# Kernel optimization log

Hardware: AMD Instinct MI355X
Metric: run time of the kernel (lower is better)

Reference implementation:

```python
import jax, jax.numpy as jnp
import numpy as np

N_NODES = 50000
N_EDGES = 800000
IN_CH, HIDDEN, OUT_CH = 128, 128, 64
EPS = 1e-5


def setup_inputs() -> dict:
    key = jax.random.key(0)
    ks = jax.random.split(key, 16)
    s = lambda fan_in: 1.0 / np.sqrt(fan_in)
    return {
        "x": jax.random.normal(ks[0], (N_NODES, IN_CH), dtype=jnp.float32),
        "edge_index": jax.random.randint(ks[1], (2, N_EDGES), 0, N_NODES, dtype=jnp.int64),
        # SAGEConv1: lin_l (neighbors, with bias), lin_r (root, no bias)
        "Wl1": jax.random.uniform(ks[2], (HIDDEN, IN_CH), jnp.float32, -s(IN_CH), s(IN_CH)),
        "bl1": jnp.zeros((HIDDEN,), jnp.float32),
        "Wr1": jax.random.uniform(ks[3], (HIDDEN, IN_CH), jnp.float32, -s(IN_CH), s(IN_CH)),
        # SAGEConv2
        "Wl2": jax.random.uniform(ks[4], (HIDDEN, HIDDEN), jnp.float32, -s(HIDDEN), s(HIDDEN)),
        "bl2": jnp.zeros((HIDDEN,), jnp.float32),
        "Wr2": jax.random.uniform(ks[5], (HIDDEN, HIDDEN), jnp.float32, -s(HIDDEN), s(HIDDEN)),
        # SAGEConv3
        "Wl3": jax.random.uniform(ks[6], (OUT_CH, HIDDEN), jnp.float32, -s(HIDDEN), s(HIDDEN)),
        "bl3": jnp.zeros((OUT_CH,), jnp.float32),
        "Wr3": jax.random.uniform(ks[7], (OUT_CH, HIDDEN), jnp.float32, -s(HIDDEN), s(HIDDEN)),
        # LayerNorms
        "g1": jnp.ones((HIDDEN,), jnp.float32),
        "beta1": jnp.zeros((HIDDEN,), jnp.float32),
        "g2": jnp.ones((HIDDEN,), jnp.float32),
        "beta2": jnp.zeros((HIDDEN,), jnp.float32),
    }


def _sage_conv(x, src, dst, n_nodes, Wl, bl, Wr):
    # mean aggregation of source features at target nodes (PyG SAGEConv, aggr='mean')
    msg = x[src]                                             # [E, C] gather
    sums = jax.ops.segment_sum(msg, dst, num_segments=n_nodes)
    cnt = jax.ops.segment_sum(jnp.ones((src.shape[0],), x.dtype), dst, num_segments=n_nodes)
    mean = sums / jnp.maximum(cnt, 1.0)[:, None]
    return mean @ Wl.T + bl + x @ Wr.T


def _layernorm(h, g, b):
    mu = jnp.mean(h, axis=-1, keepdims=True)
    var = jnp.mean(jnp.square(h - mu), axis=-1, keepdims=True)
    return (h - mu) * jax.lax.rsqrt(var + EPS) * g + b


def reference(x, edge_index, Wl1, bl1, Wr1, Wl2, bl2, Wr2, Wl3, bl3, Wr3, g1, beta1, g2, beta2):
    src, dst = edge_index[0], edge_index[1]
    n = x.shape[0]
    h = jax.nn.relu(_sage_conv(x, src, dst, n, Wl1, bl1, Wr1))
    h = _layernorm(h, g1, beta1)
    h = jax.nn.relu(_sage_conv(h, src, dst, n, Wl2, bl2, Wr2))
    h = _layernorm(h, g2, beta2)
    return _sage_conv(h, src, dst, n, Wl3, bl3, Wr3)
```

## Files before the change

kernel.cpp:

```cpp
#include <hip/hip_runtime.h>

#define NNODES 50000
#define NEDGES 800000
#define FILL_CHUNK 7168
#define FILL_NCHUNK 112
#define FILL_BLOCKS (FILL_NCHUNK * 8)
#define GEMM_BLOCKS ((NNODES + 127) / 128)
#define CAP 96

using bf16x8  = __attribute__((ext_vector_type(8))) __bf16;
using floatx4 = __attribute__((ext_vector_type(4))) float;

__device__ __forceinline__ float bf2f(unsigned short u) {
  unsigned int v = ((unsigned int)u) << 16;
  return __builtin_bit_cast(float, v);
}
__device__ __forceinline__ unsigned short f2bf(float f) {
  unsigned int u = __builtin_bit_cast(unsigned int, f);
  u += 0x7fffu + ((u >> 16) & 1u);
  return (unsigned short)(u >> 16);
}

__device__ __forceinline__ signed char enc_i8(float f) {
  float g = fminf(fmaxf(f * 32.0f, -127.0f), 127.0f);
  return (signed char)__float2int_rn(g);
}

struct WPtrs {
  const float* src[6];
  unsigned short* dst[6];
  int n[6];
};

__global__ __launch_bounds__(256) void convw_zero_kernel(WPtrs p, int* __restrict__ cnt) {
  if (blockIdx.x < 320) {
    int i = blockIdx.x * 256 + threadIdx.x;
#pragma unroll
    for (int s = 0; s < 6; ++s) {
      if (i < p.n[s]) {
        p.dst[s][i] = f2bf(p.src[s][i]);
        return;
      }
      i -= p.n[s];
    }
  } else {
    int i = (blockIdx.x - 320) * 256 + threadIdx.x;
    if (i < NNODES) cnt[i] = 0;
  }
}

__device__ __forceinline__ void fill_body(int bid, const int* __restrict__ src,
                                          const int* __restrict__ dst,
                                          int* __restrict__ cnt,
                                          int* __restrict__ bucket) {
  int p = bid & 7;
  if (p == 7) return;
  int chunk = bid >> 3;
  int e0 = chunk * FILL_CHUNK;
  int e1 = min(e0 + FILL_CHUNK, NEDGES);
  for (int base = e0 + (int)threadIdx.x * 4; base < e1; base += 256 * 4) {
    int4 d4 = *(const int4*)(dst + base);
    int4 s4 = *(const int4*)(src + base);
    if ((d4.x >> 13) == p) { int sl = atomicAdd(&cnt[d4.x], 1); bucket[(size_t)d4.x * CAP + sl] = s4.x; }
    if ((d4.y >> 13) == p) { int sl = atomicAdd(&cnt[d4.y], 1); bucket[(size_t)d4.y * CAP + sl] = s4.y; }
    if ((d4.z >> 13) == p) { int sl = atomicAdd(&cnt[d4.z], 1); bucket[(size_t)d4.z * CAP + sl] = s4.z; }
    if ((d4.w >> 13) == p) { int sl = atomicAdd(&cnt[d4.w], 1); bucket[(size_t)d4.w * CAP + sl] = s4.w; }
  }
}

__device__ __forceinline__ bf16x8 load_frag(const unsigned short* p) {
  uint4 v = *(const uint4*)p;
  return __builtin_bit_cast(bf16x8, v);
}
__device__ __forceinline__ bf16x8 cvt_frag(const float* p) {
  float4 v0 = *(const float4*)p;
  float4 v1 = *(const float4*)(p + 4);
  uint4 o;
  o.x = (unsigned int)f2bf(v0.x) | ((unsigned int)f2bf(v0.y) << 16);
  o.y = (unsigned int)f2bf(v0.z) | ((unsigned int)f2bf(v0.w) << 16);
  o.z = (unsigned int)f2bf(v1.x) | ((unsigned int)f2bf(v1.y) << 16);
  o.w = (unsigned int)f2bf(v1.z) | ((unsigned int)f2bf(v1.w) << 16);
  return __builtin_bit_cast(bf16x8, o);
}

template <int NTL, int NTR, bool F32IN>
__device__ __forceinline__ void gemm_dual_body(int bid, const void* __restrict__ Ain,
                                               const unsigned short* __restrict__ W,
                                               signed char* __restrict__ yl,
                                               unsigned short* __restrict__ yr) {
  constexpr int NT = NTL + NTR;
  int wave = threadIdx.x >> 6;
  int lane = threadIdx.x & 63;
  int quad = lane >> 4;
  int m = lane & 15;
  int row0 = bid * 128 + wave * 32;
  int ar0 = min(row0 + m, NNODES - 1);
  int ar1 = min(row0 + 16 + m, NNODES - 1);
  bf16x8 a0[4], a1[4];
#pragma unroll
  for (int kt = 0; kt < 4; ++kt) {
    if constexpr (F32IN) {
      const float* A = (const float*)Ain;
      a0[kt] = cvt_frag(A + (size_t)ar0 * 128 + quad * 8 + kt * 32);
      a1[kt] = cvt_frag(A + (size_t)ar1 * 128 + quad * 8 + kt * 32);
    } else {
      const unsigned short* A = (const unsigned short*)Ain;
      a0[kt] = load_frag(A + (size_t)ar0 * 128 + quad * 8 + kt * 32);
      a1[kt] = load_frag(A + (size_t)ar1 * 128 + quad * 8 + kt * 32);
    }
  }
#pragma unroll
  for (int t = 0; t < NT; ++t) {
    const unsigned short* wp = W + (t * 16 + m) * 128 + quad * 8;
    bf16x8 w[4];
#pragma unroll
    for (int kt = 0; kt < 4; ++kt) w[kt] = load_frag(wp + kt * 32);
    floatx4 c0 = {0.f, 0.f, 0.f, 0.f};
    floatx4 c1 = {0.f, 0.f, 0.f, 0.f};
#pragma unroll
    for (int kt = 0; kt < 4; ++kt) {
      c0 = __builtin_amdgcn_mfma_f32_16x16x32_bf16(a0[kt], w[kt], c0, 0, 0, 0);
      c1 = __builtin_amdgcn_mfma_f32_16x16x32_bf16(a1[kt], w[kt], c1, 0, 0, 0);
    }
#pragma unroll
    for (int r = 0; r < 4; ++r) {
      int g0 = row0 + quad * 4 + r;
      int g1r = g0 + 16;
      if (t < NTL) {
        int col = t * 16 + m;
        if (g0 < NNODES) yl[(size_t)g0 * (NTL * 16) + col] = enc_i8(c0[r]);
        if (g1r < NNODES) yl[(size_t)g1r * (NTL * 16) + col] = enc_i8(c1[r]);
      } else {
        int col = (t - NTL) * 16 + m;
        if (g0 < NNODES) yr[(size_t)g0 * (NTR * 16) + col] = f2bf(c0[r]);
        if (g1r < NNODES) yr[(size_t)g1r * (NTR * 16) + col] = f2bf(c1[r]);
      }
    }
  }
}

__global__ __launch_bounds__(256) void fill_gemm1_kernel(
    const int* __restrict__ src, const int* __restrict__ dst, int* __restrict__ cnt,
    int* __restrict__ bucket, const float* __restrict__ x,
    const unsigned short* __restrict__ W, signed char* __restrict__ yl,
    unsigned short* __restrict__ yr) {
  if (blockIdx.x < FILL_BLOCKS)
    fill_body(blockIdx.x, src, dst, cnt, bucket);
  else
    gemm_dual_body<8, 8, true>(blockIdx.x - FILL_BLOCKS, x, W, yl, yr);
}

template <int NTL, int NTR, bool F32IN>
__global__ __launch_bounds__(256) void gemm_dual_kernel(
    const void* __restrict__ Ain, const unsigned short* __restrict__ W,
    signed char* __restrict__ yl, unsigned short* __restrict__ yr) {
  gemm_dual_body<NTL, NTR, F32IN>(blockIdx.x, Ain, W, yl, yr);
}

#define ACCI(u, A0, A1, A2, A3)                    \
  A0 += (int)((signed char)((u) & 0xffu));         \
  A1 += (int)((signed char)(((u) >> 8) & 0xffu));  \
  A2 += (int)((signed char)(((u) >> 16) & 0xffu)); \
  A3 += (int)((signed char)((u) >> 24));

__global__ __launch_bounds__(256) void agg_ln_kernel(
    const signed char* __restrict__ yl, const unsigned short* __restrict__ yr,
    const float* __restrict__ bl, const float* __restrict__ g,
    const float* __restrict__ be, const int* __restrict__ cnt,
    const int* __restrict__ bucket, unsigned short* __restrict__ hout) {
  int gw = (blockIdx.x * blockDim.x + threadIdx.x) >> 6;
  int lane = threadIdx.x & 63;
  int qw = lane >> 4;
  int c16 = lane & 15;
  int offc = c16 * 8;
  int deg = cnt[gw];
  const int* bk = bucket + (size_t)gw * CAP;
  int a0 = 0, a1 = 0, a2 = 0, a3 = 0, a4 = 0, a5 = 0, a6 = 0, a7 = 0;
#define ACC8(v)                      \
  ACCI((v).x, a0, a1, a2, a3)        \
  ACCI((v).y, a4, a5, a6, a7)
  int e = qw;
  for (; e + 12 < deg; e += 16) {
    int i0 = bk[e], i1 = bk[e + 4], i2 = bk[e + 8], i3 = bk[e + 12];
    uint2 v0 = *(const uint2*)(yl + (size_t)i0 * 128 + offc);
    uint2 v1 = *(const uint2*)(yl + (size_t)i1 * 128 + offc);
    uint2 v2 = *(const uint2*)(yl + (size_t)i2 * 128 + offc);
    uint2 v3 = *(const uint2*)(yl + (size_t)i3 * 128 + offc);
    ACC8(v0) ACC8(v1) ACC8(v2) ACC8(v3)
  }
  for (; e + 4 < deg; e += 8) {
    int i0 = bk[e], i1 = bk[e + 4];
    uint2 v0 = *(const uint2*)(yl + (size_t)i0 * 128 + offc);
    uint2 v1 = *(const uint2*)(yl + (size_t)i1 * 128 + offc);
    ACC8(v0) ACC8(v1)
  }
  if (e < deg) {
    int i0 = bk[e];
    uint2 v = *(const uint2*)(yl + (size_t)i0 * 128 + offc);
    ACC8(v)
  }
  a0 += __shfl_xor(a0, 16); a1 += __shfl_xor(a1, 16);
  a2 += __shfl_xor(a2, 16); a3 += __shfl_xor(a3, 16);
  a4 += __shfl_xor(a4, 16); a5 += __shfl_xor(a5, 16);
  a6 += __shfl_xor(a6, 16); a7 += __shfl_xor(a7, 16);
  a0 += __shfl_xor(a0, 32); a1 += __shfl_xor(a1, 32);
  a2 += __shfl_xor(a2, 32); a3 += __shfl_xor(a3, 32);
  a4 += __shfl_xor(a4, 32); a5 += __shfl_xor(a5, 32);
  a6 += __shfl_xor(a6, 32); a7 += __shfl_xor(a7, 32);
  float idg = 0.03125f / (float)((deg > 0) ? deg : 1);
  uint4 rv = *(const uint4*)(yr + (size_t)gw * 128 + offc);
  float4 b0 = *(const float4*)(bl + offc);
  float4 b1 = *(const float4*)(bl + offc + 4);
  float x0 = (float)a0 * idg + bf2f((unsigned short)(rv.x & 0xffffu)) + b0.x;
  float x1 = (float)a1 * idg + bf2f((unsigned short)(rv.x >> 16)) + b0.y;
  float x2 = (float)a2 * idg + bf2f((unsigned short)(rv.y & 0xffffu)) + b0.z;
  float x3 = (float)a3 * idg + bf2f((unsigned short)(rv.y >> 16)) + b0.w;
  float x4 = (float)a4 * idg + bf2f((unsigned short)(rv.z & 0xffffu)) + b1.x;
  float x5 = (float)a5 * idg + bf2f((unsigned short)(rv.z >> 16)) + b1.y;
  float x6 = (float)a6 * idg + bf2f((unsigned short)(rv.w & 0xffffu)) + b1.z;
  float x7 = (float)a7 * idg + bf2f((unsigned short)(rv.w >> 16)) + b1.w;
  x0 = fmaxf(x0, 0.f); x1 = fmaxf(x1, 0.f); x2 = fmaxf(x2, 0.f); x3 = fmaxf(x3, 0.f);
  x4 = fmaxf(x4, 0.f); x5 = fmaxf(x5, 0.f); x6 = fmaxf(x6, 0.f); x7 = fmaxf(x7, 0.f);
  float sA = x0 + x1 + x2 + x3 + x4 + x5 + x6 + x7;
  float sB = x0 * x0 + x1 * x1 + x2 * x2 + x3 * x3 + x4 * x4 + x5 * x5 + x6 * x6 + x7 * x7;
#pragma unroll
  for (int msk = 1; msk < 16; msk <<= 1) {
    sA += __shfl_xor(sA, msk, 16);
    sB += __shfl_xor(sB, msk, 16);
  }
  float mu = sA * (1.0f / 128.0f);
  float var = sB * (1.0f / 128.0f) - mu * mu;
  float rs = rsqrtf(var + 1e-5f);
  float4 g0v = *(const float4*)(g + offc);
  float4 g1v = *(const float4*)(g + offc + 4);
  float4 e0v = *(const float4*)(be + offc);
  float4 e1v = *(const float4*)(be + offc + 4);
  if (qw == 0) {
    uint4 o;
    o.x = (unsigned int)f2bf((x0 - mu) * rs * g0v.x + e0v.x) |
          ((unsigned int)f2bf((x1 - mu) * rs * g0v.y + e0v.y) << 16);
    o.y = (unsigned int)f2bf((x2 - mu) * rs * g0v.z + e0v.z) |
          ((unsigned int)f2bf((x3 - mu) * rs * g0v.w + e0v.w) << 16);
    o.z = (unsigned int)f2bf((x4 - mu) * rs * g1v.x + e1v.x) |
          ((unsigned int)f2bf((x5 - mu) * rs * g1v.y + e1v.y) << 16);
    o.w = (unsigned int)f2bf((x6 - mu) * rs * g1v.z + e1v.z) |
          ((unsigned int)f2bf((x7 - mu) * rs * g1v.w + e1v.w) << 16);
    *(uint4*)(hout + (size_t)gw * 128 + offc) = o;
  }
}

__global__ __launch_bounds__(256) void agg3_kernel(
    const signed char* __restrict__ yl, const unsigned short* __restrict__ yr,
    const float* __restrict__ bl, const int* __restrict__ cnt,
    const int* __restrict__ bucket, float* __restrict__ out) {
  int gw = (blockIdx.x * blockDim.x + threadIdx.x) >> 6;
  int lane = threadIdx.x & 63;
  int ew = lane >> 3;
  int c8 = lane & 7;
  int offc = c8 * 8;
  int deg = cnt[gw];
  const int* bk = bucket + (size_t)gw * CAP;
  int a0 = 0, a1 = 0, a2 = 0, a3 = 0, a4 = 0, a5 = 0, a6 = 0, a7 = 0;
  int e = ew;
  for (; e + 8 < deg; e += 16) {
    int i0 = bk[e], i1 = bk[e + 8];
    uint2 v0 = *(const uint2*)(yl + (size_t)i0 * 64 + offc);
    uint2 v1 = *(const uint2*)(yl + (size_t)i1 * 64 + offc);
    ACC8(v0) ACC8(v1)
  }
  if (e < deg) {
    int i0 = bk[e];
    uint2 v = *(const uint2*)(yl + (size_t)i0 * 64 + offc);
    ACC8(v)
  }
#undef ACC8
  a0 += __shfl_xor(a0, 8);  a1 += __shfl_xor(a1, 8);
  a2 += __shfl_xor(a2, 8);  a3 += __shfl_xor(a3, 8);
  a4 += __shfl_xor(a4, 8);  a5 += __shfl_xor(a5, 8);
  a6 += __shfl_xor(a6, 8);  a7 += __shfl_xor(a7, 8);
  a0 += __shfl_xor(a0, 16); a1 += __shfl_xor(a1, 16);
  a2 += __shfl_xor(a2, 16); a3 += __shfl_xor(a3, 16);
  a4 += __shfl_xor(a4, 16); a5 += __shfl_xor(a5, 16);
  a6 += __shfl_xor(a6, 16); a7 += __shfl_xor(a7, 16);
  a0 += __shfl_xor(a0, 32); a1 += __shfl_xor(a1, 32);
  a2 += __shfl_xor(a2, 32); a3 += __shfl_xor(a3, 32);
  a4 += __shfl_xor(a4, 32); a5 += __shfl_xor(a5, 32);
  a6 += __shfl_xor(a6, 32); a7 += __shfl_xor(a7, 32);
  if (ew == 0) {
    float idg = 0.03125f / (float)((deg > 0) ? deg : 1);
    uint4 rv = *(const uint4*)(yr + (size_t)gw * 64 + offc);
    float4 b0 = *(const float4*)(bl + offc);
    float4 b1 = *(const float4*)(bl + offc + 4);
    float4 o0, o1;
    o0.x = (float)a0 * idg + bf2f((unsigned short)(rv.x & 0xffffu)) + b0.x;
    o0.y = (float)a1 * idg + bf2f((unsigned short)(rv.x >> 16)) + b0.y;
    o0.z = (float)a2 * idg + bf2f((unsigned short)(rv.y & 0xffffu)) + b0.z;
    o0.w = (float)a3 * idg + bf2f((unsigned short)(rv.y >> 16)) + b0.w;
    o1.x = (float)a4 * idg + bf2f((unsigned short)(rv.z & 0xffffu)) + b1.x;
    o1.y = (float)a5 * idg + bf2f((unsigned short)(rv.z >> 16)) + b1.y;
    o1.z = (float)a6 * idg + bf2f((unsigned short)(rv.w & 0xffffu)) + b1.z;
    o1.w = (float)a7 * idg + bf2f((unsigned short)(rv.w >> 16)) + b1.w;
    *(float4*)(out + (size_t)gw * 64 + offc) = o0;
    *(float4*)(out + (size_t)gw * 64 + offc + 4) = o1;
  }
}

extern "C" void kernel_launch(void* const* d_in, const int* in_sizes, int n_in,
                              void* d_out, int out_size, void* d_ws, size_t ws_size,
                              hipStream_t stream) {
  const float* x = (const float*)d_in[0];
  const int* ei = (const int*)d_in[1];
  const int* srcv = ei;
  const int* dstv = ei + NEDGES;
  const float* Wl1 = (const float*)d_in[2];
  const float* bl1 = (const float*)d_in[3];
  const float* Wr1 = (const float*)d_in[4];
  const float* Wl2 = (const float*)d_in[5];
  const float* bl2 = (const float*)d_in[6];
  const float* Wr2 = (const float*)d_in[7];
  const float* Wl3 = (const float*)d_in[8];
  const float* bl3 = (const float*)d_in[9];
  const float* Wr3 = (const float*)d_in[10];
  const float* g1 = (const float*)d_in[11];
  const float* be1 = (const float*)d_in[12];
  const float* g2 = (const float*)d_in[13];
  const float* be2 = (const float*)d_in[14];

  char* ws = (char*)d_ws;
  size_t o = 0;
  int* cnt = (int*)(ws + o);      o += 200192;
  int* bucket = (int*)(ws + o);   o += (size_t)NNODES * CAP * 4;
  unsigned short* wb1 = (unsigned short*)(ws + o); o += 65536;
  unsigned short* wb2 = (unsigned short*)(ws + o); o += 65536;
  unsigned short* wb3 = (unsigned short*)(ws + o); o += 32768;
  signed char* yl1 = (signed char*)(ws + o);       o += (size_t)50000 * 128;
  unsigned short* yr1 = (unsigned short*)(ws + o); o += (size_t)50000 * 256;
  unsigned short* h1 = (unsigned short*)(ws + o);  o += (size_t)50000 * 256;
  signed char* yl2 = (signed char*)(ws + o);       o += (size_t)50000 * 128;
  unsigned short* yr2 = (unsigned short*)(ws + o); o += (size_t)50000 * 256;
  unsigned short* h2 = (unsigned short*)(ws + o);  o += (size_t)50000 * 256;
  signed char* yl3 = (signed char*)(ws + o);       o += (size_t)50000 * 64;
  unsigned short* yr3 = (unsigned short*)(ws + o); o += (size_t)50000 * 128;

  dim3 blk(256);
  dim3 aggGrid(NNODES / 4);
  dim3 gemmGrid(GEMM_BLOCKS);

  WPtrs wp;
  wp.src[0] = Wl1; wp.dst[0] = wb1;         wp.n[0] = 128 * 128;
  wp.src[1] = Wr1; wp.dst[1] = wb1 + 16384; wp.n[1] = 128 * 128;
  wp.src[2] = Wl2; wp.dst[2] = wb2;         wp.n[2] = 128 * 128;
  wp.src[3] = Wr2; wp.dst[3] = wb2 + 16384; wp.n[3] = 128 * 128;
  wp.src[4] = Wl3; wp.dst[4] = wb3;         wp.n[4] = 64 * 128;
  wp.src[5] = Wr3; wp.dst[5] = wb3 + 8192;  wp.n[5] = 64 * 128;

  convw_zero_kernel<<<dim3(320 + 196), blk, 0, stream>>>(wp, cnt);
  fill_gemm1_kernel<<<dim3(FILL_BLOCKS + GEMM_BLOCKS), blk, 0, stream>>>(
      srcv, dstv, cnt, bucket, x, wb1, yl1, yr1);
  agg_ln_kernel<<<aggGrid, blk, 0, stream>>>(yl1, yr1, bl1, g1, be1, cnt, bucket, h1);
  gemm_dual_kernel<8, 8, false><<<gemmGrid, blk, 0, stream>>>(h1, wb2, yl2, yr2);
  agg_ln_kernel<<<aggGrid, blk, 0, stream>>>(yl2, yr2, bl2, g2, be2, cnt, bucket, h2);
  gemm_dual_kernel<4, 4, false><<<gemmGrid, blk, 0, stream>>>(h2, wb3, yl3, yr3);
  agg3_kernel<<<aggGrid, blk, 0, stream>>>(yl3, yr3, bl3, cnt, bucket, (float*)d_out);
}
```

Baseline: 287.4 us.

## Remap aggregation kernels to sub-wave groups per node with wider loads

The aggregation kernels now give each node 8 lanes (16 lanes' worth of 16-byte channel loads per thread) instead of a full wavefront, so one wave handles 8 nodes (16 in the last layer). This removes the cross-lane integer reductions over edges and the idle lanes during the LayerNorm and store phases, at the cost of serial edge loops per lane and divergence between nodes of different degree in the same wave. The fill kernel's chunk size is also halved with twice as many chunks, giving more fill blocks.

```diff
diff --git a/kernel.cpp b/kernel.cpp
--- a/kernel.cpp
+++ b/kernel.cpp
@@ -2,8 +2,8 @@
 
 #define NNODES 50000
 #define NEDGES 800000
-#define FILL_CHUNK 7168
-#define FILL_NCHUNK 112
+#define FILL_CHUNK 3584
+#define FILL_NCHUNK 224
 #define FILL_BLOCKS (FILL_NCHUNK * 8)
 #define GEMM_BLOCKS ((NNODES + 127) / 128)
 #define CAP 96
@@ -157,152 +157,134 @@
   gemm_dual_body<NTL, NTR, F32IN>(blockIdx.x, Ain, W, yl, yr);
 }
 
-#define ACCI(u, A0, A1, A2, A3)                    \
-  A0 += (int)((signed char)((u) & 0xffu));         \
-  A1 += (int)((signed char)(((u) >> 8) & 0xffu));  \
-  A2 += (int)((signed char)(((u) >> 16) & 0xffu)); \
-  A3 += (int)((signed char)((u) >> 24));
+#define ACCU(u, base)                                       \
+  a[base] += (int)((signed char)((u) & 0xffu));             \
+  a[base + 1] += (int)((signed char)(((u) >> 8) & 0xffu));  \
+  a[base + 2] += (int)((signed char)(((u) >> 16) & 0xffu)); \
+  a[base + 3] += (int)((signed char)((u) >> 24));
+#define ACC16(v) ACCU((v).x, 0) ACCU((v).y, 4) ACCU((v).z, 8) ACCU((v).w, 12)
 
 __global__ __launch_bounds__(256) void agg_ln_kernel(
     const signed char* __restrict__ yl, const unsigned short* __restrict__ yr,
     const float* __restrict__ bl, const float* __restrict__ g,
     const float* __restrict__ be, const int* __restrict__ cnt,
     const int* __restrict__ bucket, unsigned short* __restrict__ hout) {
-  int gw = (blockIdx.x * blockDim.x + threadIdx.x) >> 6;
+  int wid = (blockIdx.x * blockDim.x + threadIdx.x) >> 6;
   int lane = threadIdx.x & 63;
-  int qw = lane >> 4;
-  int c16 = lane & 15;
-  int offc = c16 * 8;
+  int grp = lane >> 3;
+  int c8 = lane & 7;
+  int gw = wid * 8 + grp;
+  if (gw >= NNODES) return;
+  int offc = c8 * 16;
   int deg = cnt[gw];
   const int* bk = bucket + (size_t)gw * CAP;
-  int a0 = 0, a1 = 0, a2 = 0, a3 = 0, a4 = 0, a5 = 0, a6 = 0, a7 = 0;
-#define ACC8(v)                      \
-  ACCI((v).x, a0, a1, a2, a3)        \
-  ACCI((v).y, a4, a5, a6, a7)
-  int e = qw;
-  for (; e + 12 < deg; e += 16) {
-    int i0 = bk[e], i1 = bk[e + 4], i2 = bk[e + 8], i3 = bk[e + 12];
-    uint2 v0 = *(const uint2*)(yl + (size_t)i0 * 128 + offc);
-    uint2 v1 = *(const uint2*)(yl + (size_t)i1 * 128 + offc);
-    uint2 v2 = *(const uint2*)(yl + (size_t)i2 * 128 + offc);
-    uint2 v3 = *(const uint2*)(yl + (size_t)i3 * 128 + offc);
-    ACC8(v0) ACC8(v1) ACC8(v2) ACC8(v3)
-  }
-  for (; e + 4 < deg; e += 8) {
-    int i0 = bk[e], i1 = bk[e + 4];
-    uint2 v0 = *(const uint2*)(yl + (size_t)i0 * 128 + offc);
-    uint2 v1 = *(const uint2*)(yl + (size_t)i1 * 128 + offc);
-    ACC8(v0) ACC8(v1)
-  }
-  if (e < deg) {
+  int a[16];
+#pragma unroll
+  for (int k = 0; k < 16; ++k) a[k] = 0;
+  int e = 0;
+  for (; e + 3 < deg; e += 4) {
+    int i0 = bk[e], i1 = bk[e + 1], i2 = bk[e + 2], i3 = bk[e + 3];
+    uint4 v0 = *(const uint4*)(yl + (size_t)i0 * 128 + offc);
+    uint4 v1 = *(const uint4*)(yl + (size_t)i1 * 128 + offc);
+    uint4 v2 = *(const uint4*)(yl + (size_t)i2 * 128 + offc);
+    uint4 v3 = *(const uint4*)(yl + (size_t)i3 * 128 + offc);
+    ACC16(v0) ACC16(v1) ACC16(v2) ACC16(v3)
+  }
+  for (; e < deg; ++e) {
     int i0 = bk[e];
-    uint2 v = *(const uint2*)(yl + (size_t)i0 * 128 + offc);
-    ACC8(v)
-  }
-  a0 += __shfl_xor(a0, 16); a1 += __shfl_xor(a1, 16);
-  a2 += __shfl_xor(a2, 16); a3 += __shfl_xor(a3, 16);
-  a4 += __shfl_xor(a4, 16); a5 += __shfl_xor(a5, 16);
-  a6 += __shfl_xor(a6, 16); a7 += __shfl_xor(a7, 16);
-  a0 += __shfl_xor(a0, 32); a1 += __shfl_xor(a1, 32);
-  a2 += __shfl_xor(a2, 32); a3 += __shfl_xor(a3, 32);
-  a4 += __shfl_xor(a4, 32); a5 += __shfl_xor(a5, 32);
-  a6 += __shfl_xor(a6, 32); a7 += __shfl_xor(a7, 32);
+    uint4 v = *(const uint4*)(yl + (size_t)i0 * 128 + offc);
+    ACC16(v)
+  }
   float idg = 0.03125f / (float)((deg > 0) ? deg : 1);
-  uint4 rv = *(const uint4*)(yr + (size_t)gw * 128 + offc);
-  float4 b0 = *(const float4*)(bl + offc);
-  float4 b1 = *(const float4*)(bl + offc + 4);
-  float x0 = (float)a0 * idg + bf2f((unsigned short)(rv.x & 0xffffu)) + b0.x;
-  float x1 = (float)a1 * idg + bf2f((unsigned short)(rv.x >> 16)) + b0.y;
-  float x2 = (float)a2 * idg + bf2f((unsigned short)(rv.y & 0xffffu)) + b0.z;
-  float x3 = (float)a3 * idg + bf2f((unsigned short)(rv.y >> 16)) + b0.w;
-  float x4 = (float)a4 * idg + bf2f((unsigned short)(rv.z & 0xffffu)) + b1.x;
-  float x5 = (float)a5 * idg + bf2f((unsigned short)(rv.z >> 16)) + b1.y;
-  float x6 = (float)a6 * idg + bf2f((unsigned short)(rv.w & 0xffffu)) + b1.z;
-  float x7 = (float)a7 * idg + bf2f((unsigned short)(rv.w >> 16)) + b1.w;
-  x0 = fmaxf(x0, 0.f); x1 = fmaxf(x1, 0.f); x2 = fmaxf(x2, 0.f); x3 = fmaxf(x3, 0.f);
-  x4 = fmaxf(x4, 0.f); x5 = fmaxf(x5, 0.f); x6 = fmaxf(x6, 0.f); x7 = fmaxf(x7, 0.f);
-  float sA = x0 + x1 + x2 + x3 + x4 + x5 + x6 + x7;
-  float sB = x0 * x0 + x1 * x1 + x2 * x2 + x3 * x3 + x4 * x4 + x5 * x5 + x6 * x6 + x7 * x7;
-#pragma unroll
-  for (int msk = 1; msk < 16; msk <<= 1) {
-    sA += __shfl_xor(sA, msk, 16);
-    sB += __shfl_xor(sB, msk, 16);
+  const unsigned short* yrp = yr + (size_t)gw * 128 + offc;
+  uint4 r0 = *(const uint4*)yrp;
+  uint4 r1 = *(const uint4*)(yrp + 8);
+  unsigned rw[8] = {r0.x, r0.y, r0.z, r0.w, r1.x, r1.y, r1.z, r1.w};
+  float blv[16], gv[16], bev[16];
+#pragma unroll
+  for (int k = 0; k < 4; ++k) {
+    *(float4*)&blv[k * 4] = *(const float4*)(bl + offc + k * 4);
+    *(float4*)&gv[k * 4] = *(const float4*)(g + offc + k * 4);
+    *(float4*)&bev[k * 4] = *(const float4*)(be + offc + k * 4);
+  }
+  float x[16], sA = 0.f, sB = 0.f;
+#pragma unroll
+  for (int k = 0; k < 16; ++k) {
+    float rv = bf2f((unsigned short)((rw[k >> 1] >> ((k & 1) * 16)) & 0xffffu));
+    float xv = (float)a[k] * idg + rv + blv[k];
+    xv = fmaxf(xv, 0.f);
+    x[k] = xv;
+    sA += xv;
+    sB += xv * xv;
+  }
+#pragma unroll
+  for (int msk = 1; msk < 8; msk <<= 1) {
+    sA += __shfl_xor(sA, msk, 8);
+    sB += __shfl_xor(sB, msk, 8);
   }
   float mu = sA * (1.0f / 128.0f);
   float var = sB * (1.0f / 128.0f) - mu * mu;
   float rs = rsqrtf(var + 1e-5f);
-  float4 g0v = *(const float4*)(g + offc);
-  float4 g1v = *(const float4*)(g + offc + 4);
-  float4 e0v = *(const float4*)(be + offc);
-  float4 e1v = *(const float4*)(be + offc + 4);
-  if (qw == 0) {
-    uint4 o;
-    o.x = (unsigned int)f2bf((x0 - mu) * rs * g0v.x + e0v.x) |
-          ((unsigned int)f2bf((x1 - mu) * rs * g0v.y + e0v.y) << 16);
-    o.y = (unsigned int)f2bf((x2 - mu) * rs * g0v.z + e0v.z) |
-          ((unsigned int)f2bf((x3 - mu) * rs * g0v.w + e0v.w) << 16);
-    o.z = (unsigned int)f2bf((x4 - mu) * rs * g1v.x + e1v.x) |
-          ((unsigned int)f2bf((x5 - mu) * rs * g1v.y + e1v.y) << 16);
-    o.w = (unsigned int)f2bf((x6 - mu) * rs * g1v.z + e1v.z) |
-          ((unsigned int)f2bf((x7 - mu) * rs * g1v.w + e1v.w) << 16);
-    *(uint4*)(hout + (size_t)gw * 128 + offc) = o;
-  }
+  unsigned ow[8];
+#pragma unroll
+  for (int k = 0; k < 8; ++k) {
+    float y0 = (x[2 * k] - mu) * rs * gv[2 * k] + bev[2 * k];
+    float y1 = (x[2 * k + 1] - mu) * rs * gv[2 * k + 1] + bev[2 * k + 1];
+    ow[k] = (unsigned)f2bf(y0) | ((unsigned)f2bf(y1) << 16);
+  }
+  uint4* op = (uint4*)(hout + (size_t)gw * 128 + offc);
+  op[0] = make_uint4(ow[0], ow[1], ow[2], ow[3]);
+  op[1] = make_uint4(ow[4], ow[5], ow[6], ow[7]);
 }
 
 __global__ __launch_bounds__(256) void agg3_kernel(
     const signed char* __restrict__ yl, const unsigned short* __restrict__ yr,
     const float* __restrict__ bl, const int* __restrict__ cnt,
     const int* __restrict__ bucket, float* __restrict__ out) {
-  int gw = (blockIdx.x * blockDim.x + threadIdx.x) >> 6;
+  int wid = (blockIdx.x * blockDim.x + threadIdx.x) >> 6;
   int lane = threadIdx.x & 63;
-  int ew = lane >> 3;
-  int c8 = lane & 7;
-  int offc = c8 * 8;
+  int grp = lane >> 2;
+  int c4 = lane & 3;
+  int gw = wid * 16 + grp;
+  if (gw >= NNODES) return;
+  int offc = c4 * 16;
   int deg = cnt[gw];
   const int* bk = bucket + (size_t)gw * CAP;
-  int a0 = 0, a1 = 0, a2 = 0, a3 = 0, a4 = 0, a5 = 0, a6 = 0, a7 = 0;
-  int e = ew;
-  for (; e + 8 < deg; e += 16) {
-    int i0 = bk[e], i1 = bk[e + 8];
-    uint2 v0 = *(const uint2*)(yl + (size_t)i0 * 64 + offc);
-    uint2 v1 = *(const uint2*)(yl + (size_t)i1 * 64 + offc);
-    ACC8(v0) ACC8(v1)
-  }
-  if (e < deg) {
+  int a[16];
+#pragma unroll
+  for (int k = 0; k < 16; ++k) a[k] = 0;
+  int e = 0;
+  for (; e + 3 < deg; e += 4) {
+    int i0 = bk[e], i1 = bk[e + 1], i2 = bk[e + 2], i3 = bk[e + 3];
+    uint4 v0 = *(const uint4*)(yl + (size_t)i0 * 64 + offc);
+    uint4 v1 = *(const uint4*)(yl + (size_t)i1 * 64 + offc);
+    uint4 v2 = *(const uint4*)(yl + (size_t)i2 * 64 + offc);
+    uint4 v3 = *(const uint4*)(yl + (size_t)i3 * 64 + offc);
+    ACC16(v0) ACC16(v1) ACC16(v2) ACC16(v3)
+  }
+  for (; e < deg; ++e) {
     int i0 = bk[e];
-    uint2 v = *(const uint2*)(yl + (size_t)i0 * 64 + offc);
-    ACC8(v)
-  }
-#undef ACC8
-  a0 += __shfl_xor(a0, 8);  a1 += __shfl_xor(a1, 8);
-  a2 += __shfl_xor(a2, 8);  a3 += __shfl_xor(a3, 8);
-  a4 += __shfl_xor(a4, 8);  a5 += __shfl_xor(a5, 8);
-  a6 += __shfl_xor(a6, 8);  a7 += __shfl_xor(a7, 8);
-  a0 += __shfl_xor(a0, 16); a1 += __shfl_xor(a1, 16);
-  a2 += __shfl_xor(a2, 16); a3 += __shfl_xor(a3, 16);
-  a4 += __shfl_xor(a4, 16); a5 += __shfl_xor(a5, 16);
-  a6 += __shfl_xor(a6, 16); a7 += __shfl_xor(a7, 16);
-  a0 += __shfl_xor(a0, 32); a1 += __shfl_xor(a1, 32);
-  a2 += __shfl_xor(a2, 32); a3 += __shfl_xor(a3, 32);
-  a4 += __shfl_xor(a4, 32); a5 += __shfl_xor(a5, 32);
-  a6 += __shfl_xor(a6, 32); a7 += __shfl_xor(a7, 32);
-  if (ew == 0) {
-    float idg = 0.03125f / (float)((deg > 0) ? deg : 1);
-    uint4 rv = *(const uint4*)(yr + (size_t)gw * 64 + offc);
-    float4 b0 = *(const float4*)(bl + offc);
-    float4 b1 = *(const float4*)(bl + offc + 4);
-    float4 o0, o1;
-    o0.x = (float)a0 * idg + bf2f((unsigned short)(rv.x & 0xffffu)) + b0.x;
-    o0.y = (float)a1 * idg + bf2f((unsigned short)(rv.x >> 16)) + b0.y;
-    o0.z = (float)a2 * idg + bf2f((unsigned short)(rv.y & 0xffffu)) + b0.z;
-    o0.w = (float)a3 * idg + bf2f((unsigned short)(rv.y >> 16)) + b0.w;
-    o1.x = (float)a4 * idg + bf2f((unsigned short)(rv.z & 0xffffu)) + b1.x;
-    o1.y = (float)a5 * idg + bf2f((unsigned short)(rv.z >> 16)) + b1.y;
-    o1.z = (float)a6 * idg + bf2f((unsigned short)(rv.w & 0xffffu)) + b1.z;
-    o1.w = (float)a7 * idg + bf2f((unsigned short)(rv.w >> 16)) + b1.w;
-    *(float4*)(out + (size_t)gw * 64 + offc) = o0;
-    *(float4*)(out + (size_t)gw * 64 + offc + 4) = o1;
-  }
+    uint4 v = *(const uint4*)(yl + (size_t)i0 * 64 + offc);
+    ACC16(v)
+  }
+  float idg = 0.03125f / (float)((deg > 0) ? deg : 1);
+  const unsigned short* yrp = yr + (size_t)gw * 64 + offc;
+  uint4 r0 = *(const uint4*)yrp;
+  uint4 r1 = *(const uint4*)(yrp + 8);
+  unsigned rw[8] = {r0.x, r0.y, r0.z, r0.w, r1.x, r1.y, r1.z, r1.w};
+  float blv[16];
+#pragma unroll
+  for (int k = 0; k < 4; ++k)
+    *(float4*)&blv[k * 4] = *(const float4*)(bl + offc + k * 4);
+  float o[16];
+#pragma unroll
+  for (int k = 0; k < 16; ++k) {
+    float rv = bf2f((unsigned short)((rw[k >> 1] >> ((k & 1) * 16)) & 0xffffu));
+    o[k] = (float)a[k] * idg + rv + blv[k];
+  }
+  float* op = out + (size_t)gw * 64 + offc;
+#pragma unroll
+  for (int k = 0; k < 4; ++k) *(float4*)(op + k * 4) = *(float4*)&o[k * 4];
 }
 
 extern "C" void kernel_launch(void* const* d_in, const int* in_sizes, int n_in,
@@ -343,7 +325,8 @@
   unsigned short* yr3 = (unsigned short*)(ws + o); o += (size_t)50000 * 128;
 
   dim3 blk(256);
-  dim3 aggGrid(NNODES / 4);
+  dim3 aggGrid((NNODES + 31) / 32);
+  dim3 agg3Grid((NNODES + 63) / 64);
   dim3 gemmGrid(GEMM_BLOCKS);
 
   WPtrs wp;
@@ -361,5 +344,5 @@
   gemm_dual_kernel<8, 8, false><<<gemmGrid, blk, 0, stream>>>(h1, wb2, yl2, yr2);
   agg_ln_kernel<<<aggGrid, blk, 0, stream>>>(yl2, yr2, bl2, g2, be2, cnt, bucket, h2);
   gemm_dual_kernel<4, 4, false><<<gemmGrid, blk, 0, stream>>>(h2, wb3, yl3, yr3);
-  agg3_kernel<<<aggGrid, blk, 0, stream>>>(yl3, yr3, bl3, cnt, bucket, (float*)d_out);
-}
+  agg3_kernel<<<agg3Grid, blk, 0, stream>>>(yl3, yr3, bl3, cnt, bucket, (float*)d_out);
+}
```

New measurement: 267.9 us. 1.07x faster.
